# Kernel tuning notes

Hardware: AMD Instinct MI355X
Metric: run time of the kernel (lower is better)

Reference implementation:

```python
import jax, jax.numpy as jnp
import numpy as np

POOL = 7           # pool_size_after_rpn
CROP = POOL * 2    # pre_pool_size


def _crop_resize_pool(bottom, rois, im_info):
    # TF tf.image.crop_and_resize (bilinear, extrapolation_value=0) fused with 2x2 max pool
    B, H, W, C = bottom.shape
    dt = bottom.dtype
    batch_ids = rois[:, 0].astype(jnp.int32)            # [N]
    im_h, im_w = im_info[0], im_info[1]
    x1 = rois[:, 1] / im_w
    y1 = rois[:, 2] / im_h
    x2 = rois[:, 3] / im_w
    y2 = rois[:, 4] / im_h
    grid = jnp.arange(CROP, dtype=dt)
    # TF sampling grid for crop_size>1: in_y = y1*(H-1) + i*(y2-y1)*(H-1)/(crop-1)
    ys = y1[:, None] * (H - 1) + grid[None, :] * ((y2 - y1) * (H - 1) / (CROP - 1))[:, None]  # [N,ch]
    xs = x1[:, None] * (W - 1) + grid[None, :] * ((x2 - x1) * (W - 1) / (CROP - 1))[:, None]  # [N,cw]
    vy = (ys >= 0) & (ys <= H - 1)
    vx = (xs >= 0) & (xs <= W - 1)
    y0f = jnp.floor(ys)
    x0f = jnp.floor(xs)
    ly = (ys - y0f)[:, :, None, None]                   # [N,ch,1,1]
    lx = (xs - x0f)[:, None, :, None]                   # [N,1,cw,1]
    y0 = jnp.clip(y0f, 0, H - 1).astype(jnp.int32)
    y1i = jnp.clip(jnp.ceil(ys), 0, H - 1).astype(jnp.int32)
    x0 = jnp.clip(x0f, 0, W - 1).astype(jnp.int32)
    x1i = jnp.clip(jnp.ceil(xs), 0, W - 1).astype(jnp.int32)
    flat = bottom.reshape(B * H * W, C)
    base = (batch_ids * (H * W))[:, None, None]

    def g(yi, xi):
        # irregular per-box gather of corner values -> [N,ch,cw,C]
        return jnp.take(flat, base + yi[:, :, None] * W + xi[:, None, :], axis=0)

    tl, tr, bl, br = g(y0, x0), g(y0, x1i), g(y1i, x0), g(y1i, x1i)
    top = tl + (tr - tl) * lx
    bot = bl + (br - bl) * lx
    crops = top + (bot - top) * ly                      # [N,CROP,CROP,C]
    mask = (vy[:, :, None] & vx[:, None, :])[..., None]
    crops = jnp.where(mask, crops, jnp.zeros((), dt))   # extrapolation_value = 0
    N = crops.shape[0]
    # MaxPooling2D(pool_size=2, strides=2, padding='SAME'); CROP is even -> exact 2x2 blocks
    return crops.reshape(N, POOL, 2, POOL, 2, C).max(axis=(2, 4))


def setup_inputs() -> dict:
    key = jax.random.key(0)
    kb, k0, k1, k2, k3 = jax.random.split(key, 5)
    B, H, W, C, NROI = 2, 64, 64, 512, 512
    IM = 1024.0
    bottom = jax.random.normal(kb, (B, H, W, C), dtype=jnp.float32)
    bids = jax.random.randint(k0, (NROI,), 0, B).astype(jnp.float32)
    x1 = jax.random.uniform(k1, (NROI,), minval=0.0, maxval=IM - 64.0)
    y1 = jax.random.uniform(k2, (NROI,), minval=0.0, maxval=IM - 64.0)
    wh = jax.random.uniform(k3, (NROI, 2), minval=32.0, maxval=256.0)
    x2 = jnp.minimum(x1 + wh[:, 0], IM - 1.0)
    y2 = jnp.minimum(y1 + wh[:, 1], IM - 1.0)
    rois = jnp.stack([bids, x1, y1, x2, y2], axis=1)    # [N,5]: (batch_id,x1,y1,x2,y2)
    im_info = jnp.array([IM, IM], dtype=jnp.float32)    # [height, width]
    return {"bottom": bottom, "rois": rois, "im_info": im_info}


def reference(bottom, rois, im_info):
    return _crop_resize_pool(bottom, rois, im_info)
```

## Files before the change

kernel.cpp:

```cpp
#include <hip/hip_runtime.h>
#include <math.h>


constexpr int POOLSZ = 7;
constexpr int CROPSZ = 14;
constexpr int Hc = 64, Wc = 64, C4 = 128;

typedef float vfloat4 __attribute__((ext_vector_type(4)));

struct F8 { float4 lo, hi; };

__device__ __forceinline__ float4 lerp4(float4 a, float4 b, float t) {
    return make_float4(fmaf(b.x - a.x, t, a.x),
                       fmaf(b.y - a.y, t, a.y),
                       fmaf(b.z - a.z, t, a.z),
                       fmaf(b.w - a.w, t, a.w));
}
__device__ __forceinline__ F8 lerp8(const F8& a, const F8& b, float t) {
    F8 r; r.lo = lerp4(a.lo, b.lo, t); r.hi = lerp4(a.hi, b.hi, t); return r;
}
__device__ __forceinline__ float4 f4max(float4 a, float4 b) {
    return make_float4(fmaxf(a.x, b.x), fmaxf(a.y, b.y),
                       fmaxf(a.z, b.z), fmaxf(a.w, b.w));
}
__device__ __forceinline__ F8 f8max(const F8& a, const F8& b) {
    F8 r; r.lo = f4max(a.lo, b.lo); r.hi = f4max(a.hi, b.hi); return r;
}
__device__ __forceinline__ F8 mask8(const F8& v, bool ok) {
    F8 r;
    r.lo = ok ? v.lo : make_float4(0.f, 0.f, 0.f, 0.f);
    r.hi = ok ? v.hi : make_float4(0.f, 0.f, 0.f, 0.f);
    return r;
}
__device__ __forceinline__ int rfl(int x) { return __builtin_amdgcn_readfirstlane(x); }

__global__ __launch_bounds__(64, 4)
void crop_pool_kernel(const float4* __restrict__ bot4,
                      const float* __restrict__ rois,
                      const float* __restrict__ im_info,
                      float4* __restrict__ out4, int nwg)
{
    const int bid = blockIdx.x;
    const int blk = (bid & 7) * (nwg >> 3) + (bid >> 3);

    const int n  = blk / (POOLSZ * POOLSZ);
    const int p  = blk - n * (POOLSZ * POOLSZ);
    const int py = p / POOLSZ;
    const int px = p - py * POOLSZ;

    const float inv_w = 1.0f / im_info[1];
    const float inv_h = 1.0f / im_info[0];
    const float* r5 = rois + n * 5;
    const int bb = rfl((int)r5[0]);
    const float rx1 = r5[1] * inv_w, ry1 = r5[2] * inv_h;
    const float rx2 = r5[3] * inv_w, ry2 = r5[4] * inv_h;

    const float sy = (ry2 - ry1) * (float)(Hc - 1) / (float)(CROPSZ - 1);
    const float sx = (rx2 - rx1) * (float)(Wc - 1) / (float)(CROPSZ - 1);
    const float oy = ry1 * (float)(Hc - 1);
    const float ox = rx1 * (float)(Wc - 1);

    int R0, R1, R2, R3;
    float ly0, ly1; bool vy0, vy1;
    {
        const float ysa = fmaf((float)(2 * py), sy, oy);
        vy0 = (ysa >= 0.f) && (ysa <= (float)(Hc - 1));
        const float fy = floorf(ysa); ly0 = ysa - fy;
        const int y0 = (int)fminf(fmaxf(fy, 0.f), (float)(Hc - 1));
        const int y1 = (int)fminf(fmaxf(ceilf(ysa), 0.f), (float)(Hc - 1));
        R0 = rfl(((bb * Hc + y0) * Wc) * C4);
        R1 = rfl(((bb * Hc + y1) * Wc) * C4);
        const float ysb = fmaf((float)(2 * py + 1), sy, oy);
        vy1 = (ysb >= 0.f) && (ysb <= (float)(Hc - 1));
        const float fy2 = floorf(ysb); ly1 = ysb - fy2;
        const int y2 = (int)fminf(fmaxf(fy2, 0.f), (float)(Hc - 1));
        const int y3 = (int)fminf(fmaxf(ceilf(ysb), 0.f), (float)(Hc - 1));
        R2 = rfl(((bb * Hc + y2) * Wc) * C4);
        R3 = rfl(((bb * Hc + y3) * Wc) * C4);
    }
    int cA, cB, cC, cD;
    float lx0, lx1; bool vx0, vx1;
    {
        const float xsa = fmaf((float)(2 * px), sx, ox);
        vx0 = (xsa >= 0.f) && (xsa <= (float)(Wc - 1));
        const float fx = floorf(xsa); lx0 = xsa - fx;
        cA = rfl((int)fminf(fmaxf(fx, 0.f), (float)(Wc - 1)) * C4);
        cB = rfl((int)fminf(fmaxf(ceilf(xsa), 0.f), (float)(Wc - 1)) * C4);
        const float xsb = fmaf((float)(2 * px + 1), sx, ox);
        vx1 = (xsb >= 0.f) && (xsb <= (float)(Wc - 1));
        const float fx2 = floorf(xsb); lx1 = xsb - fx2;
        cC = rfl((int)fminf(fmaxf(fx2, 0.f), (float)(Wc - 1)) * C4);
        cD = rfl((int)fminf(fmaxf(ceilf(xsb), 0.f), (float)(Wc - 1)) * C4);
    }

    const int tid = threadIdx.x;

    F8 X00, X01, X10, X11, X20, X21, X30, X31;

    auto fresh = [&](int rb, F8& Xs0, F8& Xs1) {
        F8 a, b, c, d;
        a.lo = bot4[rb + cA + tid]; a.hi = bot4[rb + cA + tid + 64];
        if (cB != cA) { b.lo = bot4[rb + cB + tid]; b.hi = bot4[rb + cB + tid + 64]; }
        else b = a;
        if (cC == cA) c = a; else if (cC == cB) c = b;
        else { c.lo = bot4[rb + cC + tid]; c.hi = bot4[rb + cC + tid + 64]; }
        if (cD == cC) d = c; else if (cD == cB) d = b;
        else { d.lo = bot4[rb + cD + tid]; d.hi = bot4[rb + cD + tid + 64]; }
        Xs0 = lerp8(a, b, lx0);
        Xs1 = lerp8(c, d, lx1);
    };

    fresh(R0, X00, X01);
    if (R1 == R0)      { X10 = X00; X11 = X01; }
    else                 fresh(R1, X10, X11);
    if (R2 == R0)      { X20 = X00; X21 = X01; }
    else if (R2 == R1) { X20 = X10; X21 = X11; }
    else                 fresh(R2, X20, X21);
    if (R3 == R2)      { X30 = X20; X31 = X21; }
    else if (R3 == R1) { X30 = X10; X31 = X11; }
    else                 fresh(R3, X30, X31);

    const F8 v00 = lerp8(X00, X10, ly0);
    const F8 v01 = lerp8(X01, X11, ly0);
    const F8 v10 = lerp8(X20, X30, ly1);
    const F8 v11 = lerp8(X21, X31, ly1);

    const F8 acc = f8max(
        f8max(mask8(v00, vy0 && vx0), mask8(v01, vy0 && vx1)),
        f8max(mask8(v10, vy1 && vx0), mask8(v11, vy1 && vx1)));

    const size_t ob = (size_t)blk * C4 + tid;
    vfloat4 s0; s0.x = acc.lo.x; s0.y = acc.lo.y; s0.z = acc.lo.z; s0.w = acc.lo.w;
    vfloat4 s1; s1.x = acc.hi.x; s1.y = acc.hi.y; s1.z = acc.hi.z; s1.w = acc.hi.w;
    __builtin_nontemporal_store(s0, reinterpret_cast<vfloat4*>(&out4[ob]));
    __builtin_nontemporal_store(s1, reinterpret_cast<vfloat4*>(&out4[ob + 64]));
}

extern "C" void kernel_launch(void* const* d_in, const int* in_sizes, int n_in,
                              void* d_out, int out_size, void* d_ws, size_t ws_size,
                              hipStream_t stream) {
    const float4* bottom  = (const float4*)d_in[0];
    const float*  rois    = (const float*)d_in[1];
    const float*  im_info = (const float*)d_in[2];
    float4* out = (float4*)d_out;

    const int N = in_sizes[1] / 5;
    const int nwg = N * POOLSZ * POOLSZ;

    crop_pool_kernel<<<nwg, 64, 0, stream>>>(bottom, rois, im_info, out, nwg);
}
```

Baseline: 29.82 us.

## Sort ROIs by batch and spatial center to improve cache locality

Adds a single-block bitonic sort kernel that orders ROIs by batch id and quantized center position, then has the crop-pool kernel process ROIs in that permuted order and write each result to its original output slot. The goal is for neighbouring workgroups to touch overlapping feature-map rows so L2/MALL hit rates rise. The cost is an extra serial kernel launch with many syncthreads, plus one dependent perm load per workgroup. The existing XCD interleave of block ids may also scatter the sorted order across dies.

```diff
diff --git a/kernel.cpp b/kernel.cpp
--- a/kernel.cpp
+++ b/kernel.cpp
@@ -34,19 +34,52 @@
 }
 __device__ __forceinline__ int rfl(int x) { return __builtin_amdgcn_readfirstlane(x); }
 
+__global__ __launch_bounds__(512)
+void sort_rois_kernel(const float* __restrict__ rois, int* __restrict__ perm, int N)
+{
+    __shared__ unsigned long long s[512];
+    const int t = threadIdx.x;
+    unsigned key = 0xFFFFFFFFu;
+    if (t < N) {
+        const float* r5 = rois + t * 5;
+        const int bb = (int)r5[0];
+        const float xc = 0.5f * (r5[1] + r5[3]);
+        const float yc = 0.5f * (r5[2] + r5[4]);
+        const int yq = min(max((int)yc, 0), 1023);
+        const int xq = min(max((int)xc, 0), 1023);
+        key = ((unsigned)bb << 20) | ((unsigned)yq << 10) | (unsigned)xq;
+    }
+    s[t] = ((unsigned long long)key << 32) | (unsigned)t;
+    __syncthreads();
+    for (int k = 2; k <= 512; k <<= 1) {
+        for (int j = k >> 1; j > 0; j >>= 1) {
+            const int ixj = t ^ j;
+            if (ixj > t) {
+                const unsigned long long a = s[t], b = s[ixj];
+                const bool up = (t & k) == 0;
+                if ((up && a > b) || (!up && a < b)) { s[t] = b; s[ixj] = a; }
+            }
+            __syncthreads();
+        }
+    }
+    if (t < N) perm[t] = (int)(s[t] & 0xFFFFFFFFu);
+}
+
 __global__ __launch_bounds__(64, 4)
 void crop_pool_kernel(const float4* __restrict__ bot4,
                       const float* __restrict__ rois,
                       const float* __restrict__ im_info,
+                      const int* __restrict__ perm,
                       float4* __restrict__ out4, int nwg)
 {
     const int bid = blockIdx.x;
     const int blk = (bid & 7) * (nwg >> 3) + (bid >> 3);
 
-    const int n  = blk / (POOLSZ * POOLSZ);
-    const int p  = blk - n * (POOLSZ * POOLSZ);
+    const int nlog = blk / (POOLSZ * POOLSZ);
+    const int p    = blk - nlog * (POOLSZ * POOLSZ);
     const int py = p / POOLSZ;
     const int px = p - py * POOLSZ;
+    const int n = perm ? rfl(perm[nlog]) : nlog;
 
     const float inv_w = 1.0f / im_info[1];
     const float inv_h = 1.0f / im_info[0];
@@ -129,7 +162,7 @@
         f8max(mask8(v00, vy0 && vx0), mask8(v01, vy0 && vx1)),
         f8max(mask8(v10, vy1 && vx0), mask8(v11, vy1 && vx1)));
 
-    const size_t ob = (size_t)blk * C4 + tid;
+    const size_t ob = ((size_t)(n * (POOLSZ * POOLSZ) + p)) * C4 + tid;
     vfloat4 s0; s0.x = acc.lo.x; s0.y = acc.lo.y; s0.z = acc.lo.z; s0.w = acc.lo.w;
     vfloat4 s1; s1.x = acc.hi.x; s1.y = acc.hi.y; s1.z = acc.hi.z; s1.w = acc.hi.w;
     __builtin_nontemporal_store(s0, reinterpret_cast<vfloat4*>(&out4[ob]));
@@ -147,5 +180,10 @@
     const int N = in_sizes[1] / 5;
     const int nwg = N * POOLSZ * POOLSZ;
 
-    crop_pool_kernel<<<nwg, 64, 0, stream>>>(bottom, rois, im_info, out, nwg);
+    int* perm = nullptr;
+    if (N <= 512 && ws_size >= (size_t)N * sizeof(int)) {
+        perm = (int*)d_ws;
+        sort_rois_kernel<<<1, 512, 0, stream>>>(rois, perm, N);
+    }
+    crop_pool_kernel<<<nwg, 64, 0, stream>>>(bottom, rois, im_info, perm, out, nwg);
 }
```

Measured after the change: 34.72 us. 1.16x slower.
